# Performance work log

Hardware: AMD Instinct MI355X
Metric: run time of the kernel (lower is better)

## Reference

```python
import math
import jax, jax.numpy as jnp
import numpy as np

NUM_HEAD = 16

def get_slopes(n):
    def pow2(n):
        start = 2 ** (-(2 ** (-(math.log2(n) - 3))))
        return [start * start ** i for i in range(n)]
    if math.log2(n).is_integer():
        return pow2(n)
    c = 2 ** math.floor(math.log2(n))
    return pow2(c) + get_slopes(2 * c)[0::2][: n - c]

def setup_inputs() -> dict:
    key = jax.random.key(0)
    ks = jax.random.split(key, 5)
    B, T, D = 2, 2048, 1024
    x = jax.random.normal(ks[0], (B, T, D), dtype=jnp.float32)
    Wq = jax.random.normal(ks[1], (D, D), dtype=jnp.float32) * 0.02
    Wk = jax.random.normal(ks[2], (D, D), dtype=jnp.float32) * 0.02
    Wv = jax.random.normal(ks[3], (D, D), dtype=jnp.float32) * 0.02
    Wo = jax.random.normal(ks[4], (D, D), dtype=jnp.float32) * (0.02 / math.sqrt(2 * 24))
    return {"x": x, "Wq": Wq, "Wk": Wk, "Wv": Wv, "Wo": Wo}

def reference(x, Wq, Wk, Wv, Wo):
    B, T, D = x.shape
    H = NUM_HEAD
    hd = D // H
    # projections (no bias)
    q = (x @ Wq).reshape(B, T, H, hd).transpose(0, 2, 1, 3)  # b h t d
    k = (x @ Wk).reshape(B, T, H, hd).transpose(0, 2, 1, 3)
    v = (x @ Wv).reshape(B, T, H, hd).transpose(0, 2, 1, 3)
    scores = jnp.einsum("bhqd,bhkd->bhqk", q, k) / jnp.sqrt(jnp.asarray(hd, dtype=q.dtype))
    # ALiBi bias: slopes[h] * (j - (T-1)), broadcast over query positions
    slopes = jnp.asarray(np.array(get_slopes(H), dtype=np.float32))
    alibi = slopes[:, None, None] * (jnp.arange(T, dtype=jnp.float32) - (T - 1))[None, None, :]  # h 1 k
    scores = scores + alibi[None]  # b h q k
    causal = jnp.tril(jnp.ones((T, T), dtype=bool))
    masked = jnp.where(causal[None, None], scores.astype(jnp.float32), jnp.finfo(jnp.float32).min)
    p = jax.nn.softmax(masked, axis=-1)
    attn_out = jnp.einsum("bhqk,bhkd->bhqd", p, v)
    attn_out = attn_out.transpose(0, 2, 1, 3).reshape(B, T, D)
    return attn_out @ Wo
```

## Files before the change

### kernel.cpp

```cpp
#include <hip/hip_runtime.h>
#include <hip/hip_bf16.h>
#include <math.h>

#define B_ 2
#define T_ 2048
#define D_ 1024
#define H_ 16
#define HD 64

typedef __bf16 bf16;
typedef bf16 bf16x8 __attribute__((ext_vector_type(8)));
typedef bf16 bf16x4 __attribute__((ext_vector_type(4)));
typedef short short4v __attribute__((ext_vector_type(4)));
typedef float f32x4 __attribute__((ext_vector_type(4)));

#define GL2LDS16(g, l) __builtin_amdgcn_global_load_lds(                      \
    (const __attribute__((address_space(1))) void*)(g),                       \
    (__attribute__((address_space(3))) void*)(l), 16, 0, 0)

static __device__ __forceinline__ f32x4 mfma16x16x16(bf16x4 a, bf16x4 b, f32x4 c) {
#if defined(__HIP_DEVICE_COMPILE__)
# if __has_builtin(__builtin_amdgcn_mfma_f32_16x16x16bf16_1k)
    return __builtin_amdgcn_mfma_f32_16x16x16bf16_1k(
        __builtin_bit_cast(short4v, a), __builtin_bit_cast(short4v, b), c, 0, 0, 0);
# else
    asm("v_mfma_f32_16x16x16_bf16 %0, %1, %2, %0" : "+v"(c) : "v"(a), "v"(b));
    return c;
# endif
#else
    (void)a; (void)b;
    return c;
#endif
}

static __device__ __forceinline__ bf16x4 lo4(bf16x8 v) {
    return __builtin_shufflevector(v, v, 0, 1, 2, 3);
}
static __device__ __forceinline__ bf16x4 hi4(bf16x8 v) {
    return __builtin_shufflevector(v, v, 4, 5, 6, 7);
}

__global__ __launch_bounds__(256) void prep_inputs(const float* __restrict__ x,
                                                   const float* __restrict__ W0,
                                                   const float* __restrict__ W1,
                                                   const float* __restrict__ W2,
                                                   const float* __restrict__ W3,
                                                   bf16* __restrict__ xb,
                                                   bf16* __restrict__ Wt) {
    const int z = blockIdx.z;
    const int tid = threadIdx.x;
    if (z >= 4) {
        size_t i = ((((size_t)(z - 4) * 256 + blockIdx.y * 16 + blockIdx.x) * 256) + tid) * 4;
        float4 v = *(const float4*)(x + i);
        bf16 tmp[4] = {(bf16)v.x, (bf16)v.y, (bf16)v.z, (bf16)v.w};
        *(uint2*)(xb + i) = *(const uint2*)tmp;
        return;
    }
    __shared__ bf16 tile[64 * 72];
    const float* W = (z == 0) ? W0 : (z == 1) ? W1 : (z == 2) ? W2 : W3;
    bf16* out = Wt + (size_t)z * D_ * D_;
    const int k0 = blockIdx.y * 64, n0 = blockIdx.x * 64;
    for (int it = 0; it < 4; ++it) {
        int idx = it * 256 + tid;
        int r = idx >> 4;
        int c4 = (idx & 15) << 2;
        float4 v = *(const float4*)(W + (size_t)(k0 + r) * D_ + n0 + c4);
        tile[(c4 + 0) * 72 + r] = (bf16)v.x;
        tile[(c4 + 1) * 72 + r] = (bf16)v.y;
        tile[(c4 + 2) * 72 + r] = (bf16)v.z;
        tile[(c4 + 3) * 72 + r] = (bf16)v.w;
    }
    __syncthreads();
    for (int it = 0; it < 2; ++it) {
        int idx = it * 256 + tid;
        int r = idx >> 3;
        int c8 = (idx & 7) << 3;
        bf16x8 v = *(const bf16x8*)&tile[r * 72 + c8];
        *(bf16x8*)(out + (size_t)(n0 + r) * D_ + k0 + c8) = v;
    }
}

__global__ __launch_bounds__(256) void gemm_qkv(const bf16* __restrict__ A,
                                                const bf16* __restrict__ Bt,
                                                bf16* __restrict__ Cout) {
    __shared__ bf16 As[2][2][128 * 32];
    __shared__ bf16 Bs[2][3][2][64 * 32];
    const int bid = blockIdx.x;
    const int xcd = bid & 7, rr = bid >> 3;
    const int y   = (xcd << 2) + (rr & 3);
    const int xx  = rr >> 2;
    const int m0 = y * 128, n0 = xx * 64;

    const int tid = threadIdx.x;
    const int wave = tid >> 6, lane = tid & 63;
    const int quad = lane >> 4, l16 = lane & 15;
    const int wr = wave >> 1, wc = wave & 1;

    const int lrow = lane >> 2, lcol = (lane & 3) << 3;
    const bf16* ag = A + (size_t)(m0 + wave * 32 + lrow) * D_ + lcol;
    const size_t brow = (size_t)(n0 + wave * 16 + lrow) * D_ + lcol;
    const int a_off = (wave * 32 + lrow) * 32 + lcol;
    const int b_off = (wave * 16 + lrow) * 32 + lcol;

    f32x4 acc[3][4][2];
#pragma unroll
    for (int z = 0; z < 3; ++z)
#pragma unroll
        for (int mi = 0; mi < 4; ++mi)
#pragma unroll
            for (int ni = 0; ni < 2; ++ni) acc[z][mi][ni] = (f32x4){0.f, 0.f, 0.f, 0.f};

    auto stage = [&](int buf, int kb) {
        GL2LDS16(ag + kb,                        &As[buf][0][a_off]);
        GL2LDS16(ag + (size_t)16 * D_ + kb,      &As[buf][0][a_off + 16 * 32]);
        GL2LDS16(ag + kb + 32,                   &As[buf][1][a_off]);
        GL2LDS16(ag + (size_t)16 * D_ + kb + 32, &As[buf][1][a_off + 16 * 32]);
#pragma unroll
        for (int z = 0; z < 3; ++z) {
            const bf16* bg = Bt + (size_t)z * D_ * D_ + brow;
            GL2LDS16(bg + kb,      &Bs[buf][z][0][b_off]);
            GL2LDS16(bg + kb + 32, &Bs[buf][z][1][b_off]);
        }
    };

    stage(0, 0);
    __syncthreads();
    int cur = 0;
    for (int kb = 0; kb < D_; kb += 64) {
        if (kb + 64 < D_) stage(cur ^ 1, kb + 64);
#pragma unroll
        for (int half = 0; half < 2; ++half) {
            bf16x8 af[4];
#pragma unroll
            for (int mi = 0; mi < 4; ++mi)
                af[mi] = *(const bf16x8*)&As[cur][half][(wr * 64 + mi * 16 + l16) * 32 + quad * 8];
#pragma unroll
            for (int z = 0; z < 3; ++z) {
                bf16x8 bfr[2];
#pragma unroll
                for (int ni = 0; ni < 2; ++ni)
                    bfr[ni] = *(const bf16x8*)&Bs[cur][z][half][(wc * 32 + ni * 16 + l16) * 32 + quad * 8];
                if (z < 2) {
#pragma unroll
                    for (int mi = 0; mi < 4; ++mi)
#pragma unroll
                        for (int ni = 0; ni < 2; ++ni)
                            acc[z][mi][ni] = __builtin_amdgcn_mfma_f32_16x16x32_bf16(
                                bfr[ni], af[mi], acc[z][mi][ni], 0, 0, 0);
                } else {
#pragma unroll
                    for (int mi = 0; mi < 4; ++mi)
#pragma unroll
                        for (int ni = 0; ni < 2; ++ni)
                            acc[z][mi][ni] = __builtin_amdgcn_mfma_f32_16x16x32_bf16(
                                af[mi], bfr[ni], acc[z][mi][ni], 0, 0, 0);
                }
            }
        }
        __syncthreads();
        cur ^= 1;
    }

#pragma unroll
    for (int z = 0; z < 3; ++z) {
        bf16* Cb = Cout + (size_t)z * (B_ * T_) * D_;
        const float qscale = (z == 0) ? 0.180336887f : 1.0f;
        if (z < 2) {
#pragma unroll
            for (int mi = 0; mi < 4; ++mi)
#pragma unroll
                for (int ni = 0; ni < 2; ++ni) {
                    int m = m0 + wr * 64 + mi * 16 + l16;
                    int n = n0 + wc * 32 + ni * 16 + quad * 4;
                    int b = m >> 11, t = m & (T_ - 1);
                    int h = n >> 6, d = n & (HD - 1);
                    bf16 o4[4];
                    for (int r = 0; r < 4; ++r) o4[r] = (bf16)(acc[z][mi][ni][r] * qscale);
                    *(uint2*)&Cb[(((((size_t)b * H_ + h) * T_ + t) << 6) + d)] =
                        *(const uint2*)o4;
                }
        } else {
#pragma unroll
            for (int mi = 0; mi < 4; ++mi)
#pragma unroll
                for (int ni = 0; ni < 2; ++ni) {
                    int m = m0 + wr * 64 + mi * 16 + quad * 4;
                    int n = n0 + wc * 32 + ni * 16 + l16;
                    int b = m >> 11, t = m & (T_ - 1);
                    int h = n >> 6, d = n & (HD - 1);
                    bf16 o4[4];
                    for (int r = 0; r < 4; ++r) o4[r] = (bf16)acc[z][mi][ni][r];
                    *(uint2*)&Cb[((((size_t)b * H_ + h) * HD + d) * T_ + t)] =
                        *(const uint2*)o4;
                }
        }
    }
}

__global__ __launch_bounds__(256) void gemm_out(const bf16* __restrict__ A,
                                                const bf16* __restrict__ Bt,
                                                float* __restrict__ Cout) {
    __shared__ bf16 As[2][2][128 * 32];
    __shared__ bf16 Bs[2][2][64 * 32];
    const int bid = blockIdx.x;
    const int xcd = bid & 7, rr = bid >> 3;
    const int y   = (xcd << 2) + (rr & 3);
    const int xx  = rr >> 2;
    const int m0 = y * 128, n0 = xx * 64;

    const int tid = threadIdx.x;
    const int wave = tid >> 6, lane = tid & 63;
    const int quad = lane >> 4, l16 = lane & 15;
    const int wr = wave >> 1, wc = wave & 1;

    const int lrow = lane >> 2, lcol = (lane & 3) << 3;
    const bf16* ag = A  + (size_t)(m0 + wave * 32 + lrow) * D_ + lcol;
    const bf16* bg = Bt + (size_t)(n0 + wave * 16 + lrow) * D_ + lcol;
    const int a_off = (wave * 32 + lrow) * 32 + lcol;
    const int b_off = (wave * 16 + lrow) * 32 + lcol;

    f32x4 acc[4][2];
    for (int mi = 0; mi < 4; ++mi)
        for (int ni = 0; ni < 2; ++ni) acc[mi][ni] = (f32x4){0.f, 0.f, 0.f, 0.f};

    auto stage = [&](int buf, int kb) {
        GL2LDS16(ag + kb,                        &As[buf][0][a_off]);
        GL2LDS16(ag + (size_t)16 * D_ + kb,      &As[buf][0][a_off + 16 * 32]);
        GL2LDS16(ag + kb + 32,                   &As[buf][1][a_off]);
        GL2LDS16(ag + (size_t)16 * D_ + kb + 32, &As[buf][1][a_off + 16 * 32]);
        GL2LDS16(bg + kb,                        &Bs[buf][0][b_off]);
        GL2LDS16(bg + kb + 32,                   &Bs[buf][1][b_off]);
    };

    stage(0, 0);
    __syncthreads();
    int cur = 0;
    for (int kb = 0; kb < D_; kb += 64) {
        if (kb + 64 < D_) stage(cur ^ 1, kb + 64);
#pragma unroll
        for (int half = 0; half < 2; ++half) {
            bf16x8 af[4], bfr[2];
#pragma unroll
            for (int mi = 0; mi < 4; ++mi)
                af[mi] = *(const bf16x8*)&As[cur][half][(wr * 64 + mi * 16 + l16) * 32 + quad * 8];
#pragma unroll
            for (int ni = 0; ni < 2; ++ni)
                bfr[ni] = *(const bf16x8*)&Bs[cur][half][(wc * 32 + ni * 16 + l16) * 32 + quad * 8];
#pragma unroll
            for (int mi = 0; mi < 4; ++mi)
#pragma unroll
                for (int ni = 0; ni < 2; ++ni)
                    acc[mi][ni] = __builtin_amdgcn_mfma_f32_16x16x32_bf16(
                        bfr[ni], af[mi], acc[mi][ni], 0, 0, 0);
        }
        __syncthreads();
        cur ^= 1;
    }

    for (int mi = 0; mi < 4; ++mi)
        for (int ni = 0; ni < 2; ++ni) {
            int m = m0 + wr * 64 + mi * 16 + l16;
            int n = n0 + wc * 32 + ni * 16 + quad * 4;
            *(f32x4*)&Cout[(size_t)m * D_ + n] = acc[mi][ni];
        }
}

__device__ __constant__ unsigned char ITEM_QT[24] = {
    8,9,10,11,12,13,14,15, 7,15, 6,14, 5,13, 4,12, 3,11, 2,10, 1,9, 0,8};
__device__ __constant__ unsigned char ITEM_KIND[24] = {
    1,1,1,1,1,1,1,1, 0,2, 0,2, 0,2, 0,2, 0,2, 0,2, 0,2, 0,2};

#define LDK 72
#define LDP 136

struct KVStage { bf16x8 k0, k1, v0, v1; };

__global__ __launch_bounds__(512, 4) void attn_kernel(const bf16* __restrict__ Q,
                                                      const bf16* __restrict__ K,
                                                      const bf16* __restrict__ Vt,
                                                      bf16* __restrict__ O,
                                                      float* __restrict__ Opart,
                                                      float2* __restrict__ ML) {
    __shared__ bf16 Ks[128 * LDK];
    __shared__ bf16 Vs[64 * LDP];

    const int bh = blockIdx.x;
    const int item = blockIdx.y;
    const int qt = ITEM_QT[item];
    const int kind = ITEM_KIND[item];
    const int h = bh & (H_ - 1), b = bh >> 4;
    const int tid = threadIdx.x;
    const int wave = tid >> 6, lane = tid & 63;
    const int quad = lane >> 4, l16 = lane & 15;

    const bf16* Qb = Q + (size_t)bh * T_ * HD;
    const bf16* Kb = K + (size_t)bh * T_ * HD;
    const bf16* Vb = Vt + (size_t)bh * HD * T_;

    const float slope2 = exp2f(-0.5f * (float)(h + 1)) * 1.44269504f;

    bf16x8 qf[2];
    {
        const bf16* qrow = Qb + (size_t)(qt * 128 + wave * 16 + l16) * HD + quad * 8;
        qf[0] = *(const bf16x8*)(qrow);
        qf[1] = *(const bf16x8*)(qrow + 32);
    }

    const int slot0 = tid, slot1 = 512 + tid;
    const int rk0 = slot0 >> 3, ck0 = (slot0 & 7) << 3;
    const int rk1 = slot1 >> 3, ck1 = (slot1 & 7) << 3;
    const int rv0 = slot0 >> 4, c0 = slot0 & 15;
    const int rv1 = slot1 >> 4, c1 = slot1 & 15;
    const int vs0 = rv0 * LDP + (c0 & 1) * 64 + (c0 >> 1) * 4;
    const int vs1 = rv1 * LDP + (c1 & 1) * 64 + (c1 >> 1) * 4;

    auto loadKV = [&](int t, KVStage& st) {
        const bf16* kb = Kb + (size_t)t * 128 * HD;
        st.k0 = *(const bf16x8*)(kb + rk0 * HD + ck0);
        st.k1 = *(const bf16x8*)(kb + rk1 * HD + ck1);
        const bf16* vb = Vb + t * 128;
        st.v0 = *(const bf16x8*)(vb + (size_t)rv0 * T_ + c0 * 8);
        st.v1 = *(const bf16x8*)(vb + (size_t)rv1 * T_ + c1 * 8);
    };
    auto storeKV = [&](const KVStage& st) {
        *(bf16x8*)&Ks[rk0 * LDK + ck0] = st.k0;
        *(bf16x8*)&Ks[rk1 * LDK + ck1] = st.k1;
        *(bf16x4*)&Vs[vs0]      = lo4(st.v0);
        *(bf16x4*)&Vs[vs0 + 32] = hi4(st.v0);
        *(bf16x4*)&Vs[vs1]      = lo4(st.v1);
        *(bf16x4*)&Vs[vs1 + 32] = hi4(st.v1);
    };

    f32x4 acc[4];
    for (int df = 0; df < 4; ++df) acc[df] = (f32x4){0.f, 0.f, 0.f, 0.f};
    float m_run = -INFINITY, l_lane = 0.f;

    const int qglob = qt * 128 + wave * 16 + l16;
    const int nkt = qt + 1;
    const int kt0 = (kind == 2) ? 8 : 0;
    const int kt1 = (kind == 1) ? 8 : nkt;

    auto compute = [&](int kt, bool last) {
        f32x4 s[8];
#pragma unroll
        for (int nf = 0; nf < 8; ++nf) {
            bf16x8 kf0 = *(const bf16x8*)&Ks[(nf * 16 + l16) * LDK + quad * 8];
            bf16x8 kf1 = *(const bf16x8*)&Ks[(nf * 16 + l16) * LDK + 32 + quad * 8];
            f32x4 zz = (f32x4){0.f, 0.f, 0.f, 0.f};
            __builtin_amdgcn_s_setprio(1);
            zz = __builtin_amdgcn_mfma_f32_16x16x32_bf16(kf0, qf[0], zz, 0, 0, 0);
            zz = __builtin_amdgcn_mfma_f32_16x16x32_bf16(kf1, qf[1], zz, 0, 0, 0);
            __builtin_amdgcn_s_setprio(0);
            s[nf] = zz;
        }

        const float j0f = (float)(kt * 128 + quad * 4 - (T_ - 1));
#pragma unroll
        for (int nf = 0; nf < 8; ++nf)
#pragma unroll
            for (int r = 0; r < 4; ++r)
                s[nf][r] += slope2 * (j0f + (float)(nf * 16 + r));
        if (last) {
            const int jb = kt * 128 + quad * 4;
#pragma unroll
            for (int nf = 0; nf < 8; ++nf)
#pragma unroll
                for (int r = 0; r < 4; ++r)
                    if (jb + nf * 16 + r > qglob) s[nf][r] = -INFINITY;
        }

        float a[8];
#pragma unroll
        for (int nf = 0; nf < 8; ++nf)
            a[nf] = fmaxf(fmaxf(s[nf][0], s[nf][1]), fmaxf(s[nf][2], s[nf][3]));
        float t0 = fmaxf(a[0], a[1]), t1 = fmaxf(a[2], a[3]);
        float t2 = fmaxf(a[4], a[5]), t3 = fmaxf(a[6], a[7]);
        float mx = fmaxf(fmaxf(t0, t1), fmaxf(t2, t3));
        mx = fmaxf(mx, __shfl_xor(mx, 16, 64));
        mx = fmaxf(mx, __shfl_xor(mx, 32, 64));

        if (!__all(mx - m_run <= 8.f)) {
            const float mnew = fmaxf(m_run, mx);
            const float alpha = exp2f(m_run - mnew);
            l_lane *= alpha;
#pragma unroll
            for (int df = 0; df < 4; ++df) acc[df] *= alpha;
            m_run = mnew;
        }

        float rs0 = 0.f, rs1 = 0.f;
        bf16x4 pf[8];
#pragma unroll
        for (int nf = 0; nf < 8; ++nf) {
            float p0 = exp2f(s[nf][0] - m_run);
            float p1 = exp2f(s[nf][1] - m_run);
            float p2 = exp2f(s[nf][2] - m_run);
            float p3 = exp2f(s[nf][3] - m_run);
            if (nf & 1) rs1 += (p0 + p1) + (p2 + p3);
            else        rs0 += (p0 + p1) + (p2 + p3);
            pf[nf] = (bf16x4){(bf16)p0, (bf16)p1, (bf16)p2, (bf16)p3};
        }
        l_lane += rs0 + rs1;

#pragma unroll
        for (int j = 0; j < 4; ++j) {
            bf16x8 w[4];
#pragma unroll
            for (int df = 0; df < 4; ++df)
                w[df] = *(const bf16x8*)&Vs[(df * 16 + l16) * LDP + quad * 32 + j * 8];
            __builtin_amdgcn_s_setprio(1);
#pragma unroll
            for (int df = 0; df < 4; ++df) {
                acc[df] = mfma16x16x16(lo4(w[df]), pf[2 * j],     acc[df]);
                acc[df] = mfma16x16x16(hi4(w[df]), pf[2 * j + 1], acc[df]);
            }
            __builtin_amdgcn_s_setprio(0);
        }
    };

    KVStage sA, sB;
    loadKV(kt0, sA);
    int kt = kt0;
    for (;;) {
        __syncthreads();
        storeKV(sA);
        if (kt + 1 < kt1) loadKV(kt + 1, sB);
        __syncthreads();
        compute(kt, kt == nkt - 1);
        if (++kt >= kt1) break;
        __syncthreads();
        storeKV(sB);
        if (kt + 1 < kt1) loadKV(kt + 1, sA);
        __syncthreads();
        compute(kt, kt == nkt - 1);
        if (++kt >= kt1) break;
    }

    float l_run = l_lane;
    l_run += __shfl_xor(l_run, 16, 64);
    l_run += __shfl_xor(l_run, 32, 64);

    if (kind == 0) {
        const float inv = 1.0f / l_run;
        for (int df = 0; df < 4; ++df) {
            bf16 o4[4];
            for (int r = 0; r < 4; ++r) o4[r] = (bf16)(acc[df][r] * inv);
            *(uint2*)&O[(((size_t)b * T_ + qglob) * H_ + h) * HD + df * 16 + quad * 4] =
                *(const uint2*)o4;
        }
    } else {
        const int pidx = (bh * 8 + (qt - 8)) * 2 + (kind == 2 ? 1 : 0);
        const int ql = wave * 16 + l16;
        float* dst = Opart + (size_t)pidx * 8192 + ql * 64;
        for (int df = 0; df < 4; ++df)
            *(f32x4*)&dst[df * 16 + quad * 4] = acc[df];
        if (quad == 0) ML[pidx * 128 + ql] = make_float2(m_run, l_run);
    }
}

__global__ __launch_bounds__(512) void attn_merge(const float* __restrict__ Opart,
                                                  const float2* __restrict__ ML,
                                                  bf16* __restrict__ O) {
    const int qt = 8 + blockIdx.x, bh = blockIdx.y;
    const int h = bh & (H_ - 1), b = bh >> 4;
    const int tid = threadIdx.x;
    const int q = tid >> 2, dc = (tid & 3) << 4;
    const int p0 = (bh * 8 + blockIdx.x) * 2, p1 = p0 + 1;

    const float2 ml0 = ML[p0 * 128 + q], ml1 = ML[p1 * 128 + q];
    const float M = fmaxf(ml0.x, ml1.x);
    const float e0 = exp2f(ml0.x - M), e1 = exp2f(ml1.x - M);
    const float inv = 1.0f / (e0 * ml0.y + e1 * ml1.y);

    const float* a = Opart + (size_t)p0 * 8192 + q * 64 + dc;
    const float* c = Opart + (size_t)p1 * 8192 + q * 64 + dc;
    bf16 o16[16];
    for (int j = 0; j < 4; ++j) {
        f32x4 va = *(const f32x4*)(a + j * 4);
        f32x4 vc = *(const f32x4*)(c + j * 4);
        for (int r = 0; r < 4; ++r)
            o16[j * 4 + r] = (bf16)((va[r] * e0 + vc[r] * e1) * inv);
    }
    const int t = qt * 128 + q;
    bf16* dst = O + (((size_t)b * T_ + t) * H_ + h) * HD + dc;
    *(bf16x8*)dst = *(const bf16x8*)o16;
    *(bf16x8*)(dst + 8) = *(const bf16x8*)(o16 + 8);
}

extern "C" void kernel_launch(void* const* d_in, const int* in_sizes, int n_in,
                              void* d_out, int out_size, void* d_ws, size_t ws_size,
                              hipStream_t stream) {
    const float* x  = (const float*)d_in[0];
    const float* Wq = (const float*)d_in[1];
    const float* Wk = (const float*)d_in[2];
    const float* Wv = (const float*)d_in[3];
    const float* Wo = (const float*)d_in[4];
    float* out = (float*)d_out;

    const size_t M = (size_t)B_ * T_;
    const size_t XE = M * D_;
    const size_t WE = (size_t)D_ * D_;

    char* ws = (char*)d_ws;
    size_t off = 0;
    auto carve = [&](size_t bytes) {
        void* p = ws + off;
        off += (bytes + 255) & ~(size_t)255;
        return p;
    };
    bf16* xb  = (bf16*)carve(XE * 2);
    bf16* Wt  = (bf16*)carve(4 * WE * 2);
    bf16* QKV = (bf16*)carve(3 * XE * 2);
    float*  Opart = (float*)carve(32 * 8 * 2 * 8192 * sizeof(float));
    float2* MLbuf = (float2*)carve(32 * 8 * 2 * 128 * sizeof(float2));
    bf16* attn = xb;

    prep_inputs<<<dim3(16, 16, 20), 256, 0, stream>>>(x, Wq, Wk, Wv, Wo, xb, Wt);

    gemm_qkv<<<512, 256, 0, stream>>>(xb, Wt, QKV);
    attn_kernel<<<dim3(32, 24), 512, 0, stream>>>(QKV, QKV + XE, QKV + 2 * XE,
                                                  attn, Opart, MLbuf);
    attn_merge<<<dim3(8, 32), 512, 0, stream>>>(Opart, MLbuf, attn);
    gemm_out<<<512, 256, 0, stream>>>(attn, Wt + 3 * WE, out);
}
```

Measured before the change: 189.5 us.

## Stream K tiles directly into double-buffered LDS via global_load_lds

K tiles now go from global memory straight into a double-buffered, split-half LDS layout using global_load_lds DMA. This replaces the old path of loading into registers and then writing to LDS. The next tile's K and V loads are issued after the barrier, so they overlap with compute on the current buffer. This cuts VGPR staging and ds_write traffic for K, at the cost of more LDS (two K buffers), which may affect occupancy. Correctness also depends on barriers waiting for the asynchronous LDS writes to finish.

```diff
diff --git a/kernel.cpp b/kernel.cpp
--- a/kernel.cpp
+++ b/kernel.cpp
@@ -270,10 +270,9 @@
 __device__ __constant__ unsigned char ITEM_KIND[24] = {
     1,1,1,1,1,1,1,1, 0,2, 0,2, 0,2, 0,2, 0,2, 0,2, 0,2, 0,2};
 
-#define LDK 72
 #define LDP 136
 
-struct KVStage { bf16x8 k0, k1, v0, v1; };
+struct VStage { bf16x8 v0, v1; };
 
 __global__ __launch_bounds__(512, 4) void attn_kernel(const bf16* __restrict__ Q,
                                                       const bf16* __restrict__ K,
@@ -281,7 +280,7 @@
                                                       bf16* __restrict__ O,
                                                       float* __restrict__ Opart,
                                                       float2* __restrict__ ML) {
-    __shared__ bf16 Ks[128 * LDK];
+    __shared__ bf16 Kh[2][2][128 * 32];
     __shared__ bf16 Vs[64 * LDP];
 
     const int bh = blockIdx.x;
@@ -306,25 +305,24 @@
         qf[1] = *(const bf16x8*)(qrow + 32);
     }
 
+    auto stageK = [&](int buf, int t) {
+        const bf16* kg = Kb + ((size_t)t * 128 + (tid >> 2)) * HD + ((tid & 3) << 3);
+        GL2LDS16(kg,      &Kh[buf][0][tid * 8]);
+        GL2LDS16(kg + 32, &Kh[buf][1][tid * 8]);
+    };
+
     const int slot0 = tid, slot1 = 512 + tid;
-    const int rk0 = slot0 >> 3, ck0 = (slot0 & 7) << 3;
-    const int rk1 = slot1 >> 3, ck1 = (slot1 & 7) << 3;
     const int rv0 = slot0 >> 4, c0 = slot0 & 15;
     const int rv1 = slot1 >> 4, c1 = slot1 & 15;
     const int vs0 = rv0 * LDP + (c0 & 1) * 64 + (c0 >> 1) * 4;
     const int vs1 = rv1 * LDP + (c1 & 1) * 64 + (c1 >> 1) * 4;
 
-    auto loadKV = [&](int t, KVStage& st) {
-        const bf16* kb = Kb + (size_t)t * 128 * HD;
-        st.k0 = *(const bf16x8*)(kb + rk0 * HD + ck0);
-        st.k1 = *(const bf16x8*)(kb + rk1 * HD + ck1);
+    auto loadV = [&](int t, VStage& st) {
         const bf16* vb = Vb + t * 128;
         st.v0 = *(const bf16x8*)(vb + (size_t)rv0 * T_ + c0 * 8);
         st.v1 = *(const bf16x8*)(vb + (size_t)rv1 * T_ + c1 * 8);
     };
-    auto storeKV = [&](const KVStage& st) {
-        *(bf16x8*)&Ks[rk0 * LDK + ck0] = st.k0;
-        *(bf16x8*)&Ks[rk1 * LDK + ck1] = st.k1;
+    auto storeV = [&](const VStage& st) {
         *(bf16x4*)&Vs[vs0]      = lo4(st.v0);
         *(bf16x4*)&Vs[vs0 + 32] = hi4(st.v0);
         *(bf16x4*)&Vs[vs1]      = lo4(st.v1);
@@ -340,12 +338,12 @@
     const int kt0 = (kind == 2) ? 8 : 0;
     const int kt1 = (kind == 1) ? 8 : nkt;
 
-    auto compute = [&](int kt, bool last) {
+    auto compute = [&](int kt, int buf, bool last) {
         f32x4 s[8];
 #pragma unroll
         for (int nf = 0; nf < 8; ++nf) {
-            bf16x8 kf0 = *(const bf16x8*)&Ks[(nf * 16 + l16) * LDK + quad * 8];
-            bf16x8 kf1 = *(const bf16x8*)&Ks[(nf * 16 + l16) * LDK + 32 + quad * 8];
+            bf16x8 kf0 = *(const bf16x8*)&Kh[buf][0][(nf * 16 + l16) * 32 + quad * 8];
+            bf16x8 kf1 = *(const bf16x8*)&Kh[buf][1][(nf * 16 + l16) * 32 + quad * 8];
             f32x4 zz = (f32x4){0.f, 0.f, 0.f, 0.f};
             __builtin_amdgcn_s_setprio(1);
             zz = __builtin_amdgcn_mfma_f32_16x16x32_bf16(kf0, qf[0], zz, 0, 0, 0);
@@ -418,21 +416,22 @@
         }
     };
 
-    KVStage sA, sB;
-    loadKV(kt0, sA);
+    VStage sA, sB;
+    stageK(0, kt0);
+    loadV(kt0, sA);
     int kt = kt0;
     for (;;) {
         __syncthreads();
-        storeKV(sA);
-        if (kt + 1 < kt1) loadKV(kt + 1, sB);
+        storeV(sA);
         __syncthreads();
-        compute(kt, kt == nkt - 1);
+        if (kt + 1 < kt1) { stageK(1, kt + 1); loadV(kt + 1, sB); }
+        compute(kt, 0, kt == nkt - 1);
         if (++kt >= kt1) break;
         __syncthreads();
-        storeKV(sB);
-        if (kt + 1 < kt1) loadKV(kt + 1, sA);
+        storeV(sB);
         __syncthreads();
-        compute(kt, kt == nkt - 1);
+        if (kt + 1 < kt1) { stageK(0, kt + 1); loadV(kt + 1, sA); }
+        compute(kt, 1, kt == nkt - 1);
         if (++kt >= kt1) break;
     }
 
```

After: 182.8 us. -3.5%, faster.
